# Optimization experiments

Hardware: AMD Instinct MI355X
Metric: run time of the kernel (lower is better)

The kernel has to match this reference:

```python
import jax, jax.numpy as jnp
import numpy as np

D_MODEL = 1024
H = 16
D_HEAD = D_MODEL // H


def setup_inputs() -> dict:
    key = jax.random.key(0)
    ks = jax.random.split(key, 9)
    B, S = 2, 2048
    x = jax.random.normal(ks[0], (B, S, D_MODEL), dtype=jnp.float32)
    s = 1.0 / np.sqrt(D_HEAD)
    # per-head Q/K/V linears, stacked: W[h, out, in], b[h, out] (torch Linear: y = x W^T + b)
    Wq = jax.random.normal(ks[1], (H, D_HEAD, D_HEAD), dtype=jnp.float32) * s
    bq = jax.random.normal(ks[2], (H, D_HEAD), dtype=jnp.float32) * 0.01
    Wk = jax.random.normal(ks[3], (H, D_HEAD, D_HEAD), dtype=jnp.float32) * s
    bk = jax.random.normal(ks[4], (H, D_HEAD), dtype=jnp.float32) * 0.01
    Wv = jax.random.normal(ks[5], (H, D_HEAD, D_HEAD), dtype=jnp.float32) * s
    bv = jax.random.normal(ks[6], (H, D_HEAD), dtype=jnp.float32) * 0.01
    Wo = jax.random.normal(ks[7], (D_MODEL, D_MODEL), dtype=jnp.float32) / np.sqrt(D_MODEL)
    bo = jax.random.normal(ks[8], (D_MODEL,), dtype=jnp.float32) * 0.01
    return {"x": x, "Wq": Wq, "bq": bq, "Wk": Wk, "bk": bk,
            "Wv": Wv, "bv": bv, "Wo": Wo, "bo": bo}


def reference(x, Wq, bq, Wk, bk, Wv, bv, Wo, bo):
    B, S, D = x.shape
    xh = x.reshape(B, S, H, D_HEAD)  # split along feature dim, head-major
    q = jnp.einsum('bshi,hoi->bsho', xh, Wq) + bq
    k = jnp.einsum('bshi,hoi->bsho', xh, Wk) + bk
    v = jnp.einsum('bshi,hoi->bsho', xh, Wv) + bv
    scale = 1.0 / jnp.sqrt(jnp.asarray(D_HEAD, dtype=x.dtype))  # source scales by sqrt(d_model//h)
    scores = jnp.einsum('bqhd,bkhd->bhqk', q, k) * scale
    causal = jnp.tril(jnp.ones((S, S), dtype=bool))
    scores = jnp.where(causal, scores, -jnp.inf)
    attn = jax.nn.softmax(scores, axis=-1)
    out = jnp.einsum('bhqk,bkhd->bqhd', attn, v).reshape(B, S, D)
    return out @ Wo.T + bo
```

## Files before the change

kernel.cpp:

```cpp
#include <hip/hip_runtime.h>
#include <cstddef>

#define Bc 2
#define Sc 2048
#define Dc 1024
#define Hc 16
#define QSC 0.18033688011112042f

typedef short short8 __attribute__((ext_vector_type(8)));
typedef float floatx4 __attribute__((ext_vector_type(4)));
typedef unsigned short ushort_t;

#if __has_builtin(__builtin_amdgcn_exp2f)
#define EXP2F(x) __builtin_amdgcn_exp2f(x)
#else
#define EXP2F(x) exp2f(x)
#endif

__device__ __forceinline__ unsigned pack2bf(float a, float b) {
    unsigned ua = __float_as_uint(a) + 0x8000u;
    unsigned ub = __float_as_uint(b) + 0x8000u;
    return __builtin_amdgcn_perm(ub, ua, 0x07060302u);
}
__device__ __forceinline__ ushort_t f2bf(float f) {
    return (ushort_t)((__float_as_uint(f) + 0x8000u) >> 16);
}

template<int N>
__device__ __forceinline__ float row_ror(float x) {
    return __int_as_float(__builtin_amdgcn_update_dpp(
        0, __float_as_int(x), 0x120 + N, 0xF, 0xF, false));
}
__device__ __forceinline__ float rsum16(float x) {
    x += row_ror<1>(x); x += row_ror<2>(x);
    x += row_ror<4>(x); x += row_ror<8>(x);
    return x;
}

__global__ __launch_bounds__(256) void wcvt_kernel(
    const float* __restrict__ Wo, const float* __restrict__ Wq,
    const float* __restrict__ Wk, const float* __restrict__ Wv,
    ushort_t* __restrict__ WoB, ushort_t* __restrict__ Wqkvb)
{
    int idx = (blockIdx.x * 256 + threadIdx.x) * 8;
    const float* src; ushort_t* dst;
    if (idx < 1048576) { src = Wo + idx; dst = WoB + idx; }
    else {
        int r = idx - 1048576;
        int w = r >> 16, off = r & 65535;
        src = (w == 0 ? Wq : (w == 1 ? Wk : Wv)) + off;
        dst = Wqkvb + r;
    }
    float4 a = *(const float4*)src;
    float4 c = *(const float4*)(src + 4);
    uint4 o;
    o.x = pack2bf(a.x, a.y); o.y = pack2bf(a.z, a.w);
    o.z = pack2bf(c.x, c.y); o.w = pack2bf(c.z, c.w);
    *(uint4*)dst = o;
}

__global__ __launch_bounds__(256) void qkv_kernel(
    const float* __restrict__ x, const ushort_t* __restrict__ Wqkvb,
    const float* __restrict__ bq, const float* __restrict__ bk, const float* __restrict__ bv,
    ushort_t* __restrict__ Qb, ushort_t* __restrict__ Kb, ushort_t* __restrict__ VT)
{
    const int blk = blockIdx.x;
    const int st = blk & 31, h = (blk >> 5) & 15, b = blk >> 9;
    const int bh = b * Hc + h, s0 = st * 64;
    const int tid = threadIdx.x, wid = tid >> 6, lane = tid & 63;
    const int lr = lane & 15, quad = lane >> 4;

    __shared__ ushort_t Xs[64 * 72];
    __shared__ ushort_t Wsh[3 * 64 * 72];

    {
        int row = tid >> 2, cg = tid & 3;
        const float* xp = x + ((size_t)(b * Sc + s0 + row)) * Dc + h * 64 + cg * 16;
        float4 v0 = *(const float4*)xp;
        float4 v1 = *(const float4*)(xp + 4);
        float4 v2 = *(const float4*)(xp + 8);
        float4 v3 = *(const float4*)(xp + 12);
        uint4 p0, p1;
        p0.x = pack2bf(v0.x, v0.y); p0.y = pack2bf(v0.z, v0.w);
        p0.z = pack2bf(v1.x, v1.y); p0.w = pack2bf(v1.z, v1.w);
        p1.x = pack2bf(v2.x, v2.y); p1.y = pack2bf(v2.z, v2.w);
        p1.z = pack2bf(v3.x, v3.y); p1.w = pack2bf(v3.z, v3.w);
        *(uint4*)(Xs + row * 72 + cg * 16) = p0;
        *(uint4*)(Xs + row * 72 + cg * 16 + 8) = p1;
    }
    {
        const ushort_t* Wg = Wqkvb + (size_t)h * 4096;
#pragma unroll
        for (int s = 0; s < 6; ++s) {
            int c = tid + s * 256;
            int w = c >> 9, rem = c & 511, row = rem >> 3, part = rem & 7;
            *(short8*)(Wsh + (w * 64 + row) * 72 + part * 8) =
                *(const short8*)(Wg + (size_t)w * 65536 + row * 64 + part * 8);
        }
    }
    __syncthreads();

    short8 af0 = *(const short8*)(Xs + (wid * 16 + lr) * 72 + quad * 8);
    short8 af1 = *(const short8*)(Xs + (wid * 16 + lr) * 72 + 32 + quad * 8);

    const float* bias3[3] = {bq + h * 64, bk + h * 64, bv + h * 64};
    const int row = tid >> 2, cg = tid & 3;

#pragma unroll
    for (int w = 0; w < 3; ++w) {
        ushort_t* Ot = Wsh + w * 64 * 72;
        short8 bf0[4], bf1[4];
#pragma unroll
        for (int n = 0; n < 4; ++n) {
            const ushort_t* wrow = Ot + (n * 16 + lr) * 72;
            bf0[n] = *(const short8*)(wrow + quad * 8);
            bf1[n] = *(const short8*)(wrow + 32 + quad * 8);
        }
        floatx4 acc[4];
#pragma unroll
        for (int n = 0; n < 4; ++n) {
            floatx4 z = {0.f, 0.f, 0.f, 0.f};
            acc[n] = __builtin_amdgcn_mfma_f32_16x16x32_bf16(af0, bf0[n], z, 0, 0, 0);
            acc[n] = __builtin_amdgcn_mfma_f32_16x16x32_bf16(af1, bf1[n], acc[n], 0, 0, 0);
        }
        __syncthreads();
        if (w < 2) {
#pragma unroll
            for (int n = 0; n < 4; ++n) {
                float bias = bias3[w][n * 16 + lr];
#pragma unroll
                for (int r = 0; r < 4; ++r) {
                    float val = acc[n][r] + bias;
                    if (w == 0) val *= QSC;
                    Ot[(wid * 16 + quad * 4 + r) * 72 + n * 16 + lr] = f2bf(val);
                }
            }
        } else {
#pragma unroll
            for (int n = 0; n < 4; ++n) {
                float bias = bias3[2][n * 16 + lr];
                uint2 pw;
                pw.x = pack2bf(acc[n][0] + bias, acc[n][1] + bias);
                pw.y = pack2bf(acc[n][2] + bias, acc[n][3] + bias);
                *(uint2*)(Ot + (n * 16 + lr) * 72 + wid * 16 + quad * 4) = pw;
            }
        }
        __syncthreads();
        const ushort_t* srcp = Ot + row * 72 + cg * 16;
        uint4 d0 = *(const uint4*)srcp;
        uint4 d1 = *(const uint4*)(srcp + 8);
        ushort_t* dst;
        if (w == 0)      dst = Qb + ((size_t)bh * Sc + s0 + row) * 64 + cg * 16;
        else if (w == 1) dst = Kb + ((size_t)bh * Sc + s0 + row) * 64 + cg * 16;
        else             dst = VT + ((size_t)bh * 64 + row) * Sc + s0 + cg * 16;
        *(uint4*)dst = d0;
        *(uint4*)(dst + 8) = d1;
    }
}

#define ST 72

__global__ __launch_bounds__(256, 2) void attn_kernel(
    const ushort_t* __restrict__ Qg, const ushort_t* __restrict__ Kg,
    const ushort_t* __restrict__ VTg, ushort_t* __restrict__ Actx)
{
    const int blk = blockIdx.x;
    const int u = blk & 255;
    const int bh = u & 31;
    const int f = (u >> 5) & 7;
    const int tpair = (blk < 256) ? f : 15 - f;
    const int b = bh >> 4, h = bh & 15;
    const int qta = 31 - tpair, qtb = tpair;
    const int s0a = qta * 64, s0b = qtb * 64;
    const int tid = threadIdx.x, wid = tid >> 6, lane = tid & 63;
    const int lr = lane & 15, quad = lane >> 4;

    __shared__ ushort_t Ks[2][64 * ST];
    __shared__ ushort_t Vs[2][64 * ST];
    __shared__ ushort_t Ps[8 * 16 * ST];

    const ushort_t* Kbh = Kg + (size_t)bh * Sc * 64;
    const ushort_t* Vbh = VTg + (size_t)bh * 64 * Sc;

    const ushort_t* QrA = Qg + ((size_t)bh * Sc + s0a + wid * 16 + lr) * 64;
    const ushort_t* QrB = Qg + ((size_t)bh * Sc + s0b + wid * 16 + lr) * 64;
    short8 qfa0 = *(const short8*)(QrA + quad * 8);
    short8 qfa1 = *(const short8*)(QrA + 32 + quad * 8);
    short8 qfb0 = *(const short8*)(QrB + quad * 8);
    short8 qfb1 = *(const short8*)(QrB + 32 + quad * 8);

    floatx4 oA[4], oB[4];
    float lA[4], lB[4];
#pragma unroll
    for (int n = 0; n < 4; ++n) { oA[n] = floatx4{0,0,0,0}; oB[n] = floatx4{0,0,0,0}; }
#pragma unroll
    for (int r = 0; r < 4; ++r) { lA[r] = 0.f; lB[r] = 0.f; }

    const int sr0 = tid >> 3, sp0 = tid & 7;
    const int sr1 = sr0 + 32;

    short8 kr0 = *(const short8*)(Kbh + (size_t)sr0 * 64 + sp0 * 8);
    short8 kr1 = *(const short8*)(Kbh + (size_t)sr1 * 64 + sp0 * 8);
    short8 vr0 = *(const short8*)(Vbh + (size_t)sr0 * Sc + sp0 * 8);
    short8 vr1 = *(const short8*)(Vbh + (size_t)sr1 * Sc + sp0 * 8);
    *(short8*)(Ks[0] + sr0 * ST + sp0 * 8) = kr0;
    *(short8*)(Ks[0] + sr1 * ST + sp0 * 8) = kr1;
    *(short8*)(Vs[0] + sr0 * ST + sp0 * 8) = vr0;
    *(short8*)(Vs[0] + sr1 * ST + sp0 * 8) = vr1;
    __syncthreads();

    ushort_t* PwA = Ps + wid * 16 * ST;
    ushort_t* PwB = Ps + (4 + wid) * 16 * ST;

    int buf = 0;
    for (int kt = 0; kt <= qta; ++kt) {
        const bool hasB = (kt <= qtb);
        const ushort_t* Kc = Ks[buf];
        const ushort_t* Vc = Vs[buf];

        short8 kf[4][2], vf[4][2];
#pragma unroll
        for (int kg = 0; kg < 4; ++kg) {
            const ushort_t* kp = Kc + (4 * lr + kg) * ST;
            kf[kg][0] = *(const short8*)(kp + quad * 8);
            kf[kg][1] = *(const short8*)(kp + 32 + quad * 8);
        }
#pragma unroll
        for (int n = 0; n < 4; ++n) {
            const ushort_t* vp = Vc + (n * 16 + lr) * ST;
            vf[n][0] = *(const short8*)(vp + quad * 8);
            vf[n][1] = *(const short8*)(vp + 32 + quad * 8);
        }

        if (kt < qta) {
            const ushort_t* kn = Kbh + (size_t)(kt + 1) * 4096;
            const ushort_t* vn = Vbh + (kt + 1) * 64;
            kr0 = *(const short8*)(kn + (size_t)sr0 * 64 + sp0 * 8);
            kr1 = *(const short8*)(kn + (size_t)sr1 * 64 + sp0 * 8);
            vr0 = *(const short8*)(vn + (size_t)sr0 * Sc + sp0 * 8);
            vr1 = *(const short8*)(vn + (size_t)sr1 * Sc + sp0 * 8);
        }

        floatx4 sA[4], sB[4];
#pragma unroll
        for (int kg = 0; kg < 4; ++kg) {
            floatx4 z = {0.f, 0.f, 0.f, 0.f};
            floatx4 t0 = __builtin_amdgcn_mfma_f32_16x16x32_bf16(qfa0, kf[kg][0], z, 0, 0, 0);
            sA[kg] = __builtin_amdgcn_mfma_f32_16x16x32_bf16(qfa1, kf[kg][1], t0, 0, 0, 0);
        }
        if (hasB) {
#pragma unroll
            for (int kg = 0; kg < 4; ++kg) {
                floatx4 z = {0.f, 0.f, 0.f, 0.f};
                floatx4 t0 = __builtin_amdgcn_mfma_f32_16x16x32_bf16(qfb0, kf[kg][0], z, 0, 0, 0);
                sB[kg] = __builtin_amdgcn_mfma_f32_16x16x32_bf16(qfb1, kf[kg][1], t0, 0, 0, 0);
            }
        }

        if (kt == qta) {
#pragma unroll
            for (int kg = 0; kg < 4; ++kg) {
                int key = 4 * lr + kg;
#pragma unroll
                for (int r = 0; r < 4; ++r)
                    if (key > wid * 16 + quad * 4 + r) sA[kg][r] = -1e30f;
            }
        }
        if (hasB && kt == qtb) {
#pragma unroll
            for (int kg = 0; kg < 4; ++kg) {
                int key = 4 * lr + kg;
#pragma unroll
                for (int r = 0; r < 4; ++r)
                    if (key > wid * 16 + quad * 4 + r) sB[kg][r] = -1e30f;
            }
        }

#pragma unroll
        for (int r = 0; r < 4; ++r) {
            float p0 = EXP2F(sA[0][r]), p1 = EXP2F(sA[1][r]);
            float p2 = EXP2F(sA[2][r]), p3 = EXP2F(sA[3][r]);
            lA[r] += rsum16(p0 + p1 + p2 + p3);
            uint2 pw; pw.x = pack2bf(p0, p1); pw.y = pack2bf(p2, p3);
            *(uint2*)(PwA + (quad * 4 + r) * ST + 4 * lr) = pw;
        }
        if (hasB) {
#pragma unroll
            for (int r = 0; r < 4; ++r) {
                float p0 = EXP2F(sB[0][r]), p1 = EXP2F(sB[1][r]);
                float p2 = EXP2F(sB[2][r]), p3 = EXP2F(sB[3][r]);
                lB[r] += rsum16(p0 + p1 + p2 + p3);
                uint2 pw; pw.x = pack2bf(p0, p1); pw.y = pack2bf(p2, p3);
                *(uint2*)(PwB + (quad * 4 + r) * ST + 4 * lr) = pw;
            }
        }

        short8 pa0 = *(const short8*)(PwA + lr * ST + quad * 8);
        short8 pa1 = *(const short8*)(PwA + lr * ST + 32 + quad * 8);
#pragma unroll
        for (int n = 0; n < 4; ++n) {
            oA[n] = __builtin_amdgcn_mfma_f32_16x16x32_bf16(pa0, vf[n][0], oA[n], 0, 0, 0);
            oA[n] = __builtin_amdgcn_mfma_f32_16x16x32_bf16(pa1, vf[n][1], oA[n], 0, 0, 0);
        }
        if (hasB) {
            short8 pb0 = *(const short8*)(PwB + lr * ST + quad * 8);
            short8 pb1 = *(const short8*)(PwB + lr * ST + 32 + quad * 8);
#pragma unroll
            for (int n = 0; n < 4; ++n) {
                oB[n] = __builtin_amdgcn_mfma_f32_16x16x32_bf16(pb0, vf[n][0], oB[n], 0, 0, 0);
                oB[n] = __builtin_amdgcn_mfma_f32_16x16x32_bf16(pb1, vf[n][1], oB[n], 0, 0, 0);
            }
        }

        if (kt < qta) {
            *(short8*)(Ks[buf ^ 1] + sr0 * ST + sp0 * 8) = kr0;
            *(short8*)(Ks[buf ^ 1] + sr1 * ST + sp0 * 8) = kr1;
            *(short8*)(Vs[buf ^ 1] + sr0 * ST + sp0 * 8) = vr0;
            *(short8*)(Vs[buf ^ 1] + sr1 * ST + sp0 * 8) = vr1;
            buf ^= 1;
        }
        __syncthreads();
    }

#pragma unroll
    for (int r = 0; r < 4; ++r) {
        float invA = 1.f / lA[r], invB = 1.f / lB[r];
        int rowA = s0a + wid * 16 + quad * 4 + r;
        int rowB = s0b + wid * 16 + quad * 4 + r;
        ushort_t* dA = Actx + ((size_t)(b * Sc + rowA)) * Dc + h * 64 + lr;
        ushort_t* dB = Actx + ((size_t)(b * Sc + rowB)) * Dc + h * 64 + lr;
#pragma unroll
        for (int n = 0; n < 4; ++n) {
            dA[n * 16] = f2bf(oA[n][r] * invA);
            dB[n * 16] = f2bf(oB[n][r] * invB);
        }
    }
}

__global__ __launch_bounds__(256, 2) void proj_kernel(
    const ushort_t* __restrict__ Ab, const ushort_t* __restrict__ Wb,
    const float* __restrict__ bo, float* __restrict__ out)
{
    const int bn = blockIdx.x & 15, bm = blockIdx.x >> 4;
    const int tid = threadIdx.x, wid = tid >> 6, lane = tid & 63;
    const int lr = lane & 15, quad = lane >> 4;
    const int wm = wid * 32;

    __shared__ ushort_t As[128 * 40];
    __shared__ ushort_t Bs[64 * 40];

    floatx4 acc[2][4];
#pragma unroll
    for (int i = 0; i < 2; ++i)
#pragma unroll
        for (int n = 0; n < 4; ++n) acc[i][n] = floatx4{0.f, 0.f, 0.f, 0.f};

    const ushort_t* Ag = Ab + (size_t)bm * 128 * 1024;
    const ushort_t* Wg = Wb + (size_t)bn * 64 * 1024;

    const int ar0 = tid >> 2, ap0 = tid & 3;
    const int ar1 = ar0 + 64;

    short8 a0 = *(const short8*)(Ag + (size_t)ar0 * 1024 + ap0 * 8);
    short8 a1 = *(const short8*)(Ag + (size_t)ar1 * 1024 + ap0 * 8);
    short8 b0 = *(const short8*)(Wg + (size_t)ar0 * 1024 + ap0 * 8);
    *(short8*)(As + ar0 * 40 + ap0 * 8) = a0;
    *(short8*)(As + ar1 * 40 + ap0 * 8) = a1;
    *(short8*)(Bs + ar0 * 40 + ap0 * 8) = b0;
    __syncthreads();

    for (int k0 = 0; k0 < 1024; k0 += 32) {
        short8 fa0 = *(const short8*)(As + (wm + lr) * 40 + quad * 8);
        short8 fa1 = *(const short8*)(As + (wm + 16 + lr) * 40 + quad * 8);
        short8 fb[4];
#pragma unroll
        for (int n = 0; n < 4; ++n)
            fb[n] = *(const short8*)(Bs + (n * 16 + lr) * 40 + quad * 8);

        if (k0 < 992) {
            int k1 = k0 + 32;
            a0 = *(const short8*)(Ag + (size_t)ar0 * 1024 + k1 + ap0 * 8);
            a1 = *(const short8*)(Ag + (size_t)ar1 * 1024 + k1 + ap0 * 8);
            b0 = *(const short8*)(Wg + (size_t)ar0 * 1024 + k1 + ap0 * 8);
        }
#pragma unroll
        for (int n = 0; n < 4; ++n) {
            acc[0][n] = __builtin_amdgcn_mfma_f32_16x16x32_bf16(fa0, fb[n], acc[0][n], 0, 0, 0);
            acc[1][n] = __builtin_amdgcn_mfma_f32_16x16x32_bf16(fa1, fb[n], acc[1][n], 0, 0, 0);
        }
        __syncthreads();
        if (k0 < 992) {
            *(short8*)(As + ar0 * 40 + ap0 * 8) = a0;
            *(short8*)(As + ar1 * 40 + ap0 * 8) = a1;
            *(short8*)(Bs + ar0 * 40 + ap0 * 8) = b0;
            __syncthreads();
        }
    }

#pragma unroll
    for (int i = 0; i < 2; ++i) {
        int mrow = bm * 128 + wm + i * 16 + quad * 4;
#pragma unroll
        for (int n = 0; n < 4; ++n) {
            int col = bn * 64 + n * 16 + lr;
            float bias = bo[col];
#pragma unroll
            for (int r = 0; r < 4; ++r)
                out[(size_t)(mrow + r) * 1024 + col] = acc[i][n][r] + bias;
        }
    }
}

extern "C" void kernel_launch(void* const* d_in, const int* in_sizes, int n_in,
                              void* d_out, int out_size, void* d_ws, size_t ws_size,
                              hipStream_t stream)
{
    (void)in_sizes; (void)n_in; (void)out_size; (void)ws_size;
    const float* x  = (const float*)d_in[0];
    const float* Wq = (const float*)d_in[1];
    const float* bq = (const float*)d_in[2];
    const float* Wk = (const float*)d_in[3];
    const float* bk = (const float*)d_in[4];
    const float* Wv = (const float*)d_in[5];
    const float* bv = (const float*)d_in[6];
    const float* Wo = (const float*)d_in[7];
    const float* bo = (const float*)d_in[8];
    float* out = (float*)d_out;

    const size_t N4 = (size_t)Bc * Hc * Sc * 64;
    ushort_t* base  = (ushort_t*)d_ws;
    ushort_t* Qb    = base;
    ushort_t* Kb    = base + N4;
    ushort_t* VT    = base + 2 * N4;
    ushort_t* Actx  = base + 3 * N4;
    ushort_t* WoB   = base + 4 * N4;
    ushort_t* Wqkvb = base + 4 * N4 + 1048576;

    wcvt_kernel<<<dim3(608), dim3(256), 0, stream>>>(Wo, Wq, Wk, Wv, WoB, Wqkvb);
    qkv_kernel<<<dim3(Bc * Hc * (Sc / 64)), dim3(256), 0, stream>>>(
        x, Wqkvb, bq, bk, bv, Qb, Kb, VT);
    attn_kernel<<<dim3(512), dim3(256), 0, stream>>>(Qb, Kb, VT, Actx);
    proj_kernel<<<dim3(32 * 16), dim3(256), 0, stream>>>(Actx, WoB, bo, out);
}
```

Measured before the change: 146.8 us.

## Keep P in registers by computing transposed scores, dropping LDS round-trip

The attention kernel now computes S^T by swapping the MFMA operands, so each lane holds the scores for one query row and a set of keys. These map directly onto the A-operand layout of the PV MFMA. This removes the shared-memory P buffer, the store/load round-trip and the per-row DPP reductions. Row sums are accumulated per lane and reduced once with shuffles at the end. V fragments are reordered to match the new key permutation. The cost is a different key ordering that has to stay consistent between the mask, P and V, plus a few shuffles in the epilogue.

```diff
diff --git a/kernel.cpp b/kernel.cpp
--- a/kernel.cpp
+++ b/kernel.cpp
@@ -24,17 +24,6 @@
 }
 __device__ __forceinline__ ushort_t f2bf(float f) {
     return (ushort_t)((__float_as_uint(f) + 0x8000u) >> 16);
-}
-
-template<int N>
-__device__ __forceinline__ float row_ror(float x) {
-    return __int_as_float(__builtin_amdgcn_update_dpp(
-        0, __float_as_int(x), 0x120 + N, 0xF, 0xF, false));
-}
-__device__ __forceinline__ float rsum16(float x) {
-    x += row_ror<1>(x); x += row_ror<2>(x);
-    x += row_ror<4>(x); x += row_ror<8>(x);
-    return x;
 }
 
 __global__ __launch_bounds__(256) void wcvt_kernel(
@@ -177,7 +166,6 @@
 
     __shared__ ushort_t Ks[2][64 * ST];
     __shared__ ushort_t Vs[2][64 * ST];
-    __shared__ ushort_t Ps[8 * 16 * ST];
 
     const ushort_t* Kbh = Kg + (size_t)bh * Sc * 64;
     const ushort_t* Vbh = VTg + (size_t)bh * 64 * Sc;
@@ -190,11 +178,9 @@
     short8 qfb1 = *(const short8*)(QrB + 32 + quad * 8);
 
     floatx4 oA[4], oB[4];
-    float lA[4], lB[4];
+    float lA = 0.f, lB = 0.f;
 #pragma unroll
     for (int n = 0; n < 4; ++n) { oA[n] = floatx4{0,0,0,0}; oB[n] = floatx4{0,0,0,0}; }
-#pragma unroll
-    for (int r = 0; r < 4; ++r) { lA[r] = 0.f; lB[r] = 0.f; }
 
     const int sr0 = tid >> 3, sp0 = tid & 7;
     const int sr1 = sr0 + 32;
@@ -209,9 +195,6 @@
     *(short8*)(Vs[0] + sr1 * ST + sp0 * 8) = vr1;
     __syncthreads();
 
-    ushort_t* PwA = Ps + wid * 16 * ST;
-    ushort_t* PwB = Ps + (4 + wid) * 16 * ST;
-
     int buf = 0;
     for (int kt = 0; kt <= qta; ++kt) {
         const bool hasB = (kt <= qtb);
@@ -228,8 +211,8 @@
 #pragma unroll
         for (int n = 0; n < 4; ++n) {
             const ushort_t* vp = Vc + (n * 16 + lr) * ST;
-            vf[n][0] = *(const short8*)(vp + quad * 8);
-            vf[n][1] = *(const short8*)(vp + 32 + quad * 8);
+            vf[n][0] = *(const short8*)(vp + 16 * quad);
+            vf[n][1] = *(const short8*)(vp + 16 * quad + 8);
         }
 
         if (kt < qta) {
@@ -245,70 +228,72 @@
 #pragma unroll
         for (int kg = 0; kg < 4; ++kg) {
             floatx4 z = {0.f, 0.f, 0.f, 0.f};
-            floatx4 t0 = __builtin_amdgcn_mfma_f32_16x16x32_bf16(qfa0, kf[kg][0], z, 0, 0, 0);
-            sA[kg] = __builtin_amdgcn_mfma_f32_16x16x32_bf16(qfa1, kf[kg][1], t0, 0, 0, 0);
+            floatx4 t0 = __builtin_amdgcn_mfma_f32_16x16x32_bf16(kf[kg][0], qfa0, z, 0, 0, 0);
+            sA[kg] = __builtin_amdgcn_mfma_f32_16x16x32_bf16(kf[kg][1], qfa1, t0, 0, 0, 0);
         }
         if (hasB) {
 #pragma unroll
             for (int kg = 0; kg < 4; ++kg) {
                 floatx4 z = {0.f, 0.f, 0.f, 0.f};
-                floatx4 t0 = __builtin_amdgcn_mfma_f32_16x16x32_bf16(qfb0, kf[kg][0], z, 0, 0, 0);
-                sB[kg] = __builtin_amdgcn_mfma_f32_16x16x32_bf16(qfb1, kf[kg][1], t0, 0, 0, 0);
+                floatx4 t0 = __builtin_amdgcn_mfma_f32_16x16x32_bf16(kf[kg][0], qfb0, z, 0, 0, 0);
+                sB[kg] = __builtin_amdgcn_mfma_f32_16x16x32_bf16(kf[kg][1], qfb1, t0, 0, 0, 0);
             }
         }
 
+        const int qrow = wid * 16 + lr;
         if (kt == qta) {
 #pragma unroll
-            for (int kg = 0; kg < 4; ++kg) {
-                int key = 4 * lr + kg;
+            for (int kg = 0; kg < 4; ++kg)
 #pragma unroll
                 for (int r = 0; r < 4; ++r)
-                    if (key > wid * 16 + quad * 4 + r) sA[kg][r] = -1e30f;
+                    if (16 * quad + 4 * r + kg > qrow) sA[kg][r] = -1e30f;
+        }
+        if (hasB && kt == qtb) {
+#pragma unroll
+            for (int kg = 0; kg < 4; ++kg)
+#pragma unroll
+                for (int r = 0; r < 4; ++r)
+                    if (16 * quad + 4 * r + kg > qrow) sB[kg][r] = -1e30f;
+        }
+
+        {
+            float e[4][4];
+#pragma unroll
+            for (int kg = 0; kg < 4; ++kg)
+#pragma unroll
+                for (int r = 0; r < 4; ++r) e[kg][r] = EXP2F(sA[kg][r]);
+#pragma unroll
+            for (int kg = 0; kg < 4; ++kg)
+                lA += (e[kg][0] + e[kg][1]) + (e[kg][2] + e[kg][3]);
+            union { uint4 u; short8 s; } p0, p1;
+            p0.u.x = pack2bf(e[0][0], e[1][0]); p0.u.y = pack2bf(e[2][0], e[3][0]);
+            p0.u.z = pack2bf(e[0][1], e[1][1]); p0.u.w = pack2bf(e[2][1], e[3][1]);
+            p1.u.x = pack2bf(e[0][2], e[1][2]); p1.u.y = pack2bf(e[2][2], e[3][2]);
+            p1.u.z = pack2bf(e[0][3], e[1][3]); p1.u.w = pack2bf(e[2][3], e[3][3]);
+#pragma unroll
+            for (int n = 0; n < 4; ++n) {
+                oA[n] = __builtin_amdgcn_mfma_f32_16x16x32_bf16(p0.s, vf[n][0], oA[n], 0, 0, 0);
+                oA[n] = __builtin_amdgcn_mfma_f32_16x16x32_bf16(p1.s, vf[n][1], oA[n], 0, 0, 0);
             }
         }
-        if (hasB && kt == qtb) {
-#pragma unroll
-            for (int kg = 0; kg < 4; ++kg) {
-                int key = 4 * lr + kg;
-#pragma unroll
-                for (int r = 0; r < 4; ++r)
-                    if (key > wid * 16 + quad * 4 + r) sB[kg][r] = -1e30f;
-            }
-        }
-
-#pragma unroll
-        for (int r = 0; r < 4; ++r) {
-            float p0 = EXP2F(sA[0][r]), p1 = EXP2F(sA[1][r]);
-            float p2 = EXP2F(sA[2][r]), p3 = EXP2F(sA[3][r]);
-            lA[r] += rsum16(p0 + p1 + p2 + p3);
-            uint2 pw; pw.x = pack2bf(p0, p1); pw.y = pack2bf(p2, p3);
-            *(uint2*)(PwA + (quad * 4 + r) * ST + 4 * lr) = pw;
-        }
         if (hasB) {
-#pragma unroll
-            for (int r = 0; r < 4; ++r) {
-                float p0 = EXP2F(sB[0][r]), p1 = EXP2F(sB[1][r]);
-                float p2 = EXP2F(sB[2][r]), p3 = EXP2F(sB[3][r]);
-                lB[r] += rsum16(p0 + p1 + p2 + p3);
-                uint2 pw; pw.x = pack2bf(p0, p1); pw.y = pack2bf(p2, p3);
-                *(uint2*)(PwB + (quad * 4 + r) * ST + 4 * lr) = pw;
-            }
-        }
-
-        short8 pa0 = *(const short8*)(PwA + lr * ST + quad * 8);
-        short8 pa1 = *(const short8*)(PwA + lr * ST + 32 + quad * 8);
-#pragma unroll
-        for (int n = 0; n < 4; ++n) {
-            oA[n] = __builtin_amdgcn_mfma_f32_16x16x32_bf16(pa0, vf[n][0], oA[n], 0, 0, 0);
-            oA[n] = __builtin_amdgcn_mfma_f32_16x16x32_bf16(pa1, vf[n][1], oA[n], 0, 0, 0);
-        }
-        if (hasB) {
-            short8 pb0 = *(const short8*)(PwB + lr * ST + quad * 8);
-            short8 pb1 = *(const short8*)(PwB + lr * ST + 32 + quad * 8);
+            float e[4][4];
+#pragma unroll
+            for (int kg = 0; kg < 4; ++kg)
+#pragma unroll
+                for (int r = 0; r < 4; ++r) e[kg][r] = EXP2F(sB[kg][r]);
+#pragma unroll
+            for (int kg = 0; kg < 4; ++kg)
+                lB += (e[kg][0] + e[kg][1]) + (e[kg][2] + e[kg][3]);
+            union { uint4 u; short8 s; } p0, p1;
+            p0.u.x = pack2bf(e[0][0], e[1][0]); p0.u.y = pack2bf(e[2][0], e[3][0]);
+            p0.u.z = pack2bf(e[0][1], e[1][1]); p0.u.w = pack2bf(e[2][1], e[3][1]);
+            p1.u.x = pack2bf(e[0][2], e[1][2]); p1.u.y = pack2bf(e[2][2], e[3][2]);
+            p1.u.z = pack2bf(e[0][3], e[1][3]); p1.u.w = pack2bf(e[2][3], e[3][3]);
 #pragma unroll
             for (int n = 0; n < 4; ++n) {
-                oB[n] = __builtin_amdgcn_mfma_f32_16x16x32_bf16(pb0, vf[n][0], oB[n], 0, 0, 0);
-                oB[n] = __builtin_amdgcn_mfma_f32_16x16x32_bf16(pb1, vf[n][1], oB[n], 0, 0, 0);
+                oB[n] = __builtin_amdgcn_mfma_f32_16x16x32_bf16(p0.s, vf[n][0], oB[n], 0, 0, 0);
+                oB[n] = __builtin_amdgcn_mfma_f32_16x16x32_bf16(p1.s, vf[n][1], oB[n], 0, 0, 0);
             }
         }
 
@@ -322,17 +307,21 @@
         __syncthreads();
     }
 
+    lA += __shfl_xor(lA, 16, 64); lA += __shfl_xor(lA, 32, 64);
+    lB += __shfl_xor(lB, 16, 64); lB += __shfl_xor(lB, 32, 64);
+    float invA = 1.f / lA, invB = 1.f / lB;
 #pragma unroll
     for (int r = 0; r < 4; ++r) {
-        float invA = 1.f / lA[r], invB = 1.f / lB[r];
+        float iA = __shfl(invA, 4 * quad + r, 64);
+        float iB = __shfl(invB, 4 * quad + r, 64);
         int rowA = s0a + wid * 16 + quad * 4 + r;
         int rowB = s0b + wid * 16 + quad * 4 + r;
         ushort_t* dA = Actx + ((size_t)(b * Sc + rowA)) * Dc + h * 64 + lr;
         ushort_t* dB = Actx + ((size_t)(b * Sc + rowB)) * Dc + h * 64 + lr;
 #pragma unroll
         for (int n = 0; n < 4; ++n) {
-            dA[n * 16] = f2bf(oA[n][r] * invA);
-            dB[n * 16] = f2bf(oB[n][r] * invB);
+            dA[n * 16] = f2bf(oA[n][r] * iA);
+            dB[n * 16] = f2bf(oB[n][r] * iB);
         }
     }
 }
```

Result: faster. 143.5 us (-2.3%).
